# Kernel tuning notes

Measured on AMD Instinct MI355X. Metric: run time of the kernel, lower is better.

## Reference

```python
import jax, jax.numpy as jnp
import numpy as np

# Production-scale dims: tokens T = B*S = 1024, d_model = 768, 8 experts, top-2 routing
B, S, D, E, K = 1, 1024, 768, 8, 2
H = 4 * D  # expert hidden dim


def setup_inputs() -> dict:
    key = jax.random.key(0)
    ks = jax.random.split(key, 6)
    s = jnp.float32(0.02)
    return {
        "x": jax.random.normal(ks[0], (B, S, D), jnp.float32),
        "Wr": jax.random.normal(ks[1], (E, D), jnp.float32) * s,      # router Linear (no bias), torch layout [out,in]
        "W1": jax.random.normal(ks[2], (E, H, D), jnp.float32) * s,   # per-expert first Linear
        "b1": jnp.zeros((E, H), jnp.float32),
        "W2": jax.random.normal(ks[3], (E, D, H), jnp.float32) * s,   # per-expert second Linear
        "b2": jnp.zeros((E, D), jnp.float32),
        "sW1": jax.random.normal(ks[4], (H, D), jnp.float32) * s,     # shared expert
        "sb1": jnp.zeros((H,), jnp.float32),
        "sW2": jax.random.normal(ks[5], (D, H), jnp.float32) * s,
        "sb2": jnp.zeros((D,), jnp.float32),
    }


def reference(x, Wr, W1, b1, W2, b2, sW1, sb1, sW2, sb2):
    Bx, Sx, Dx = x.shape
    xf = x.reshape(-1, Dx)                                   # [T, D]
    T = xf.shape[0]

    # Router: top-k logits, others masked to -inf, then softmax.
    # softmax over -inf-masked logits == softmax over the k kept logits scattered back.
    logits = xf @ Wr.T                                       # [T, E]
    topv, idx = jax.lax.top_k(logits, K)                     # [T, K]
    gate_k = jax.nn.softmax(topv, axis=-1)                   # [T, K]
    gates = jnp.zeros((T, logits.shape[-1]), x.dtype).at[
        jnp.arange(T)[:, None], idx
    ].add(gate_k)                                            # [T, E], zero for unrouted experts

    # Expert MLPs (dense over experts; gate is exactly zero for unrouted -> same math
    # as the original masked gather/scatter loop). Dropout is identity in eval mode.
    h = jax.nn.relu(jnp.einsum('td,ehd->teh', xf, W1) + b1)  # [T, E, H]
    y = jnp.einsum('teh,edh->ted', h, W2) + b2               # [T, E, D]
    moe = jnp.einsum('te,ted->td', gates, y)                 # [T, D]

    # Shared expert: original adds 0.1 * shared(x) once per expert that selected the
    # token; every token is selected by exactly K (distinct top-k) experts.
    sh = jax.nn.relu(xf @ sW1.T + sb1) @ sW2.T + sb2         # [T, D]
    out = moe + (0.1 * K) * sh
    return out.reshape(Bx, Sx, Dx)
```

## Files before the change

kernel.cpp:

```cpp
#include <hip/hip_runtime.h>

#define T_TOK 1024
#define Dm 768
#define Hm 3072
#define NE 8
#define NPACK 3072
#define MAXTILES 32

typedef __attribute__((ext_vector_type(8))) short short8;
typedef __attribute__((ext_vector_type(4))) float f32x4;

__device__ __forceinline__ unsigned f2bf(float f) {
  unsigned u = __builtin_bit_cast(unsigned, f);
  u += 0x7fffu + ((u >> 16) & 1u);
  return u >> 16;
}
__device__ __forceinline__ unsigned pk2bf(float a, float b) {
  return f2bf(a) | (f2bf(b) << 16);
}
__device__ __forceinline__ float bf2f(unsigned short s) {
  unsigned u = ((unsigned)s) << 16;
  return __builtin_bit_cast(float, u);
}

__global__ __launch_bounds__(256) void router_kernel(
    const float* __restrict__ x, const float* __restrict__ Wr,
    int* __restrict__ counts, int* __restrict__ tlist,
    int4* __restrict__ tok2row, float2* __restrict__ tok2g) {
  __shared__ float sWr[NE * Dm];
  for (int i = threadIdx.x; i < NE * Dm; i += 256) sWr[i] = Wr[i];
  __syncthreads();
  const int wave = threadIdx.x >> 6, lane = threadIdx.x & 63;
  const int t = blockIdx.x * 4 + wave;
  float acc[NE];
#pragma unroll
  for (int e = 0; e < NE; e++) acc[e] = 0.f;
  for (int d = lane; d < Dm; d += 64) {
    float xv = x[t * Dm + d];
#pragma unroll
    for (int e = 0; e < NE; e++) acc[e] += xv * sWr[e * Dm + d];
  }
#pragma unroll
  for (int e = 0; e < NE; e++) {
#pragma unroll
    for (int off = 32; off > 0; off >>= 1) acc[e] += __shfl_down(acc[e], off);
  }
  if (lane == 0) {
    int i0 = 0; float v0 = acc[0];
#pragma unroll
    for (int e = 1; e < NE; e++) if (acc[e] > v0) { v0 = acc[e]; i0 = e; }
    int i1 = -1; float v1 = -1e30f;
#pragma unroll
    for (int e = 0; e < NE; e++) if (e != i0 && acc[e] > v1) { v1 = acc[e]; i1 = e; }
    float g0 = 1.f / (1.f + expf(v1 - v0));
    float g1 = 1.f - g0;
    int p0 = atomicAdd(&counts[i0], 1);
    tlist[i0 * T_TOK + p0] = t;
    int p1 = atomicAdd(&counts[i1], 1);
    tlist[i1 * T_TOK + p1] = t;
    tok2row[t] = make_int4(i0, p0, i1, p1);
    tok2g[t] = float2{g0, g1};
  }
}

template <int MODE>
__global__ __launch_bounds__(512) void moe_gemm(
    const float* __restrict__ x,
    const float* __restrict__ W1, const float* __restrict__ b1,
    const float* __restrict__ sW1, const float* __restrict__ sb1,
    const float* __restrict__ W2, const float* __restrict__ sW2,
    const float* __restrict__ sb2,
    unsigned short* __restrict__ hbuf, unsigned short* __restrict__ ybuf,
    float* __restrict__ outp,
    const int* __restrict__ counts, const int* __restrict__ tlist) {
  constexpr int BN    = (MODE == 0) ? 128 : 96;
  constexpr int Kfull = (MODE == 0) ? Dm : Hm;
  constexpr int NK    = Kfull / 64;
  constexpr int M_REP = (MODE == 0) ? 4 : 2;
  constexpr int N_REP = (MODE == 0) ? 2 : 3;
  constexpr int NBR   = BN / 32;

  const int b = blockIdx.x;
  int nIdx, ti;
  if constexpr (MODE == 0) { nIdx = (b % 8) + 8 * ((b / 8) % 3); ti = b / 24; }
  else                     { nIdx = b % 8;                        ti = b / 8;  }
  const int n0 = nIdx * BN;

  int e = 0, m0 = 0, pbase = 0, Ne = 0;
  bool found = false;
  for (int ee = 0; ee <= NE; ee++) {
    int ne = (ee < NE) ? counts[ee] : T_TOK;
    int nt = (ne + 127) >> 7;
    if (!found) {
      if (ti < nt) { e = ee; Ne = ne; m0 = ti << 7; found = true; }
      else { ti -= nt; pbase += ne; }
    }
  }
  if (!found) return;

  const float* Bw;
  const float* bias;
  if constexpr (MODE == 0) {
    Bw   = (e < NE) ? W1 + (size_t)e * Hm * Dm : sW1;
    bias = (e < NE) ? b1 + (size_t)e * Hm : sb1;
  } else {
    Bw   = (e < NE) ? W2 + (size_t)e * Dm * Hm : sW2;
    bias = sb2;
  }

  __shared__ unsigned short sA[128][72];
  __shared__ unsigned short sB[BN][72];

  const int tid = threadIdx.x;
  const int lane = tid & 63;
  const int wid = tid >> 6;
  int rb, cb;
  if constexpr (MODE == 0) { rb = (wid >> 2) * 64; cb = (wid & 3) * 32; }
  else                     { rb = (wid >> 1) * 32; cb = (wid & 1) * 48; }

  const float* aPtrF[4];
  const unsigned short* aPtrH[2];
  if constexpr (MODE == 0) {
#pragma unroll
    for (int c = 0; c < 4; c++) {
      int gi = m0 + c * 32 + (tid >> 4);
      int si = gi < Ne ? gi : Ne - 1;
      int tok = (e < NE) ? tlist[e * T_TOK + si] : si;
      aPtrF[c] = x + (size_t)tok * Dm + (tid & 15) * 4;
    }
  } else {
#pragma unroll
    for (int c = 0; c < 2; c++) {
      int prow = pbase + m0 + c * 64 + (tid >> 3);
      if (prow >= NPACK) prow = NPACK - 1;
      aPtrH[c] = hbuf + (size_t)prow * Hm + (tid & 7) * 8;
    }
  }
  const float* bPtrF[NBR];
#pragma unroll
  for (int c = 0; c < NBR; c++) {
    int nrow = n0 + c * 32 + (tid >> 4);
    bPtrF[c] = Bw + (size_t)nrow * Kfull + (tid & 15) * 4;
  }

  f32x4 acc[M_REP][N_REP];
#pragma unroll
  for (int m = 0; m < M_REP; m++)
#pragma unroll
    for (int n = 0; n < N_REP; n++) acc[m][n] = (f32x4)0.0f;

  const int rF = tid >> 4;
  const int cF = (tid & 15) * 4;
  const int rH = tid >> 3;
  const int cH = (tid & 7) * 8;
  const int frow = lane & 15;
  const int fk = (lane >> 4) * 8;

  float4 aFA[4], bFA[NBR], aFB[4], bFB[NBR];
  uint4 aHA[2], aHB[2];

  auto stage_load_A = [&](int ko) {
    if constexpr (MODE == 0) {
#pragma unroll
      for (int c = 0; c < 4; c++) aFA[c] = *(const float4*)(aPtrF[c] + ko);
    } else {
#pragma unroll
      for (int c = 0; c < 2; c++) aHA[c] = *(const uint4*)(aPtrH[c] + ko);
    }
#pragma unroll
    for (int c = 0; c < NBR; c++) bFA[c] = *(const float4*)(bPtrF[c] + ko);
  };
  auto stage_load_B = [&](int ko) {
    if constexpr (MODE == 0) {
#pragma unroll
      for (int c = 0; c < 4; c++) aFB[c] = *(const float4*)(aPtrF[c] + ko);
    } else {
#pragma unroll
      for (int c = 0; c < 2; c++) aHB[c] = *(const uint4*)(aPtrH[c] + ko);
    }
#pragma unroll
    for (int c = 0; c < NBR; c++) bFB[c] = *(const float4*)(bPtrF[c] + ko);
  };
  auto stage_write_A = [&]() {
    if constexpr (MODE == 0) {
#pragma unroll
      for (int c = 0; c < 4; c++)
        *(uint2*)&sA[c * 32 + rF][cF] =
            make_uint2(pk2bf(aFA[c].x, aFA[c].y), pk2bf(aFA[c].z, aFA[c].w));
    } else {
#pragma unroll
      for (int c = 0; c < 2; c++) *(uint4*)&sA[c * 64 + rH][cH] = aHA[c];
    }
#pragma unroll
    for (int c = 0; c < NBR; c++)
      *(uint2*)&sB[c * 32 + rF][cF] =
          make_uint2(pk2bf(bFA[c].x, bFA[c].y), pk2bf(bFA[c].z, bFA[c].w));
  };
  auto stage_write_B = [&]() {
    if constexpr (MODE == 0) {
#pragma unroll
      for (int c = 0; c < 4; c++)
        *(uint2*)&sA[c * 32 + rF][cF] =
            make_uint2(pk2bf(aFB[c].x, aFB[c].y), pk2bf(aFB[c].z, aFB[c].w));
    } else {
#pragma unroll
      for (int c = 0; c < 2; c++) *(uint4*)&sA[c * 64 + rH][cH] = aHB[c];
    }
#pragma unroll
    for (int c = 0; c < NBR; c++)
      *(uint2*)&sB[c * 32 + rF][cF] =
          make_uint2(pk2bf(bFB[c].x, bFB[c].y), pk2bf(bFB[c].z, bFB[c].w));
  };
  auto do_mfma = [&]() {
#pragma unroll
    for (int kk = 0; kk < 2; kk++) {
      short8 af[M_REP], bfr[N_REP];
#pragma unroll
      for (int m = 0; m < M_REP; m++)
        af[m] = *(const short8*)&sA[rb + m * 16 + frow][kk * 32 + fk];
#pragma unroll
      for (int n = 0; n < N_REP; n++)
        bfr[n] = *(const short8*)&sB[cb + n * 16 + frow][kk * 32 + fk];
#pragma unroll
      for (int m = 0; m < M_REP; m++)
#pragma unroll
        for (int n = 0; n < N_REP; n++)
          acc[m][n] = __builtin_amdgcn_mfma_f32_16x16x32_bf16(af[m], bfr[n], acc[m][n], 0, 0, 0);
    }
  };

  stage_load_A(0);
  stage_load_B(64);

  for (int ks = 0; ks < NK; ks += 2) {
    stage_write_A();
    __syncthreads();
    if (ks + 2 < NK) stage_load_A((ks + 2) * 64);
    do_mfma();
    __syncthreads();
    stage_write_B();
    __syncthreads();
    if (ks + 3 < NK) stage_load_B((ks + 3) * 64);
    do_mfma();
    __syncthreads();
  }

#pragma unroll
  for (int m = 0; m < M_REP; m++) {
    int lr = rb + m * 16 + (lane >> 4) * 4;
#pragma unroll
    for (int n = 0; n < N_REP; n++) {
      int gc = n0 + cb + n * 16 + (lane & 15);
#pragma unroll
      for (int j = 0; j < 4; j++) {
        int gi = m0 + lr + j;
        if (gi >= Ne) continue;
        float v = acc[m][n][j];
        if constexpr (MODE == 0) {
          v += bias[gc];
          v = v > 0.f ? v : 0.f;
          hbuf[(size_t)(pbase + gi) * Hm + gc] = (unsigned short)f2bf(v);
        } else {
          if (e < NE) {
            ybuf[(size_t)(pbase + gi) * Dm + gc] = (unsigned short)f2bf(v);
          } else {
            outp[(size_t)gi * Dm + gc] = 0.2f * (v + bias[gc]);
          }
        }
      }
    }
  }
}

__global__ __launch_bounds__(256) void finalize_kernel(
    const unsigned short* __restrict__ ybuf, const int* __restrict__ counts,
    const int4* __restrict__ tok2row, const float2* __restrict__ tok2g,
    const float* __restrict__ b2, float* __restrict__ out) {
  const int t = blockIdx.x;
  int bases[NE];
  int s = 0;
#pragma unroll
  for (int e = 0; e < NE; e++) { bases[e] = s; s += counts[e]; }
  const int4 rr = tok2row[t];
  const float2 gg = tok2g[t];
  const int r0 = bases[rr.x] + rr.y;
  const int r1 = bases[rr.z] + rr.w;
  for (int d = threadIdx.x; d < Dm; d += 256) {
    float v0 = bf2f(ybuf[(size_t)r0 * Dm + d]) + b2[rr.x * Dm + d];
    float v1 = bf2f(ybuf[(size_t)r1 * Dm + d]) + b2[rr.z * Dm + d];
    out[(size_t)t * Dm + d] += gg.x * v0 + gg.y * v1;
  }
}

extern "C" void kernel_launch(void* const* d_in, const int* in_sizes, int n_in,
                              void* d_out, int out_size, void* d_ws, size_t ws_size,
                              hipStream_t stream) {
  const float* x   = (const float*)d_in[0];
  const float* Wr  = (const float*)d_in[1];
  const float* W1  = (const float*)d_in[2];
  const float* b1  = (const float*)d_in[3];
  const float* W2  = (const float*)d_in[4];
  const float* b2  = (const float*)d_in[5];
  const float* sW1 = (const float*)d_in[6];
  const float* sb1 = (const float*)d_in[7];
  const float* sW2 = (const float*)d_in[8];
  const float* sb2 = (const float*)d_in[9];
  float* out = (float*)d_out;

  char* ws = (char*)d_ws;
  int*    counts  = (int*)(ws + 0);
  int4*   tok2row = (int4*)(ws + 128);
  float2* tok2g   = (float2*)(ws + 16512);
  int*    tlist   = (int*)(ws + 24704);
  unsigned short* hbuf = (unsigned short*)(ws + 57472);
  unsigned short* ybuf = (unsigned short*)(ws + 18931840);

  (void)hipMemsetAsync(counts, 0, 128, stream);

  router_kernel<<<dim3(T_TOK / 4), 256, 0, stream>>>(x, Wr, counts, tlist, tok2row, tok2g);

  moe_gemm<0><<<dim3(24 * MAXTILES), 512, 0, stream>>>(
      x, W1, b1, sW1, sb1, W2, sW2, sb2, hbuf, ybuf, out, counts, tlist);
  moe_gemm<1><<<dim3(8 * MAXTILES), 512, 0, stream>>>(
      x, W1, b1, sW1, sb1, W2, sW2, sb2, hbuf, ybuf, out, counts, tlist);

  finalize_kernel<<<dim3(T_TOK), 256, 0, stream>>>(ybuf, counts, tok2row, tok2g, b2, out);
}
```

Baseline: 356.6 us.

## Double-buffer LDS tiles in MoE GEMM to halve barriers per k-step

Shared-memory A/B tiles become two ping-pong buffers, so the next tile can be written to LDS while the current one is consumed by MFMA. Each k-tile now needs one barrier instead of two. A custom barrier macro waits only on LDS counters and adds a scheduling fence. LDS usage doubles, which may lower occupancy, and the hand-written waitcnt barrier relies on global loads being consumed before the LDS writes.

```diff
diff --git a/kernel.cpp b/kernel.cpp
--- a/kernel.cpp
+++ b/kernel.cpp
@@ -22,6 +22,13 @@
   unsigned u = ((unsigned)s) << 16;
   return __builtin_bit_cast(float, u);
 }
+
+#define SYNCB()                                            \
+  do {                                                     \
+    asm volatile("s_waitcnt lgkmcnt(0)" ::: "memory");     \
+    __builtin_amdgcn_s_barrier();                          \
+    __builtin_amdgcn_sched_barrier(0);                     \
+  } while (0)
 
 __global__ __launch_bounds__(256) void router_kernel(
     const float* __restrict__ x, const float* __restrict__ Wr,
@@ -75,7 +82,7 @@
     const int* __restrict__ counts, const int* __restrict__ tlist) {
   constexpr int BN    = (MODE == 0) ? 128 : 96;
   constexpr int Kfull = (MODE == 0) ? Dm : Hm;
-  constexpr int NK    = Kfull / 64;
+  constexpr int NT    = Kfull / 64;
   constexpr int M_REP = (MODE == 0) ? 4 : 2;
   constexpr int N_REP = (MODE == 0) ? 2 : 3;
   constexpr int NBR   = BN / 32;
@@ -108,8 +115,8 @@
     bias = sb2;
   }
 
-  __shared__ unsigned short sA[128][72];
-  __shared__ unsigned short sB[BN][72];
+  __shared__ unsigned short sA[2][128][72];
+  __shared__ unsigned short sB[2][BN][72];
 
   const int tid = threadIdx.x;
   const int lane = tid & 63;
@@ -159,7 +166,8 @@
   float4 aFA[4], bFA[NBR], aFB[4], bFB[NBR];
   uint4 aHA[2], aHB[2];
 
-  auto stage_load_A = [&](int ko) {
+  auto loadA = [&](int kt) {
+    int ko = kt * 64;
     if constexpr (MODE == 0) {
 #pragma unroll
       for (int c = 0; c < 4; c++) aFA[c] = *(const float4*)(aPtrF[c] + ko);
@@ -170,7 +178,8 @@
 #pragma unroll
     for (int c = 0; c < NBR; c++) bFA[c] = *(const float4*)(bPtrF[c] + ko);
   };
-  auto stage_load_B = [&](int ko) {
+  auto loadB = [&](int kt) {
+    int ko = kt * 64;
     if constexpr (MODE == 0) {
 #pragma unroll
       for (int c = 0; c < 4; c++) aFB[c] = *(const float4*)(aPtrF[c] + ko);
@@ -181,46 +190,46 @@
 #pragma unroll
     for (int c = 0; c < NBR; c++) bFB[c] = *(const float4*)(bPtrF[c] + ko);
   };
-  auto stage_write_A = [&]() {
+  auto writeLdsA = [&](int buf) {
     if constexpr (MODE == 0) {
 #pragma unroll
       for (int c = 0; c < 4; c++)
-        *(uint2*)&sA[c * 32 + rF][cF] =
+        *(uint2*)&sA[buf][c * 32 + rF][cF] =
             make_uint2(pk2bf(aFA[c].x, aFA[c].y), pk2bf(aFA[c].z, aFA[c].w));
     } else {
 #pragma unroll
-      for (int c = 0; c < 2; c++) *(uint4*)&sA[c * 64 + rH][cH] = aHA[c];
+      for (int c = 0; c < 2; c++) *(uint4*)&sA[buf][c * 64 + rH][cH] = aHA[c];
     }
 #pragma unroll
     for (int c = 0; c < NBR; c++)
-      *(uint2*)&sB[c * 32 + rF][cF] =
+      *(uint2*)&sB[buf][c * 32 + rF][cF] =
           make_uint2(pk2bf(bFA[c].x, bFA[c].y), pk2bf(bFA[c].z, bFA[c].w));
   };
-  auto stage_write_B = [&]() {
+  auto writeLdsB = [&](int buf) {
     if constexpr (MODE == 0) {
 #pragma unroll
       for (int c = 0; c < 4; c++)
-        *(uint2*)&sA[c * 32 + rF][cF] =
+        *(uint2*)&sA[buf][c * 32 + rF][cF] =
             make_uint2(pk2bf(aFB[c].x, aFB[c].y), pk2bf(aFB[c].z, aFB[c].w));
     } else {
 #pragma unroll
-      for (int c = 0; c < 2; c++) *(uint4*)&sA[c * 64 + rH][cH] = aHB[c];
+      for (int c = 0; c < 2; c++) *(uint4*)&sA[buf][c * 64 + rH][cH] = aHB[c];
     }
 #pragma unroll
     for (int c = 0; c < NBR; c++)
-      *(uint2*)&sB[c * 32 + rF][cF] =
+      *(uint2*)&sB[buf][c * 32 + rF][cF] =
           make_uint2(pk2bf(bFB[c].x, bFB[c].y), pk2bf(bFB[c].z, bFB[c].w));
   };
-  auto do_mfma = [&]() {
+  auto do_mfma = [&](int buf) {
 #pragma unroll
     for (int kk = 0; kk < 2; kk++) {
       short8 af[M_REP], bfr[N_REP];
 #pragma unroll
       for (int m = 0; m < M_REP; m++)
-        af[m] = *(const short8*)&sA[rb + m * 16 + frow][kk * 32 + fk];
+        af[m] = *(const short8*)&sA[buf][rb + m * 16 + frow][kk * 32 + fk];
 #pragma unroll
       for (int n = 0; n < N_REP; n++)
-        bfr[n] = *(const short8*)&sB[cb + n * 16 + frow][kk * 32 + fk];
+        bfr[n] = *(const short8*)&sB[buf][cb + n * 16 + frow][kk * 32 + fk];
 #pragma unroll
       for (int m = 0; m < M_REP; m++)
 #pragma unroll
@@ -229,20 +238,22 @@
     }
   };
 
-  stage_load_A(0);
-  stage_load_B(64);
-
-  for (int ks = 0; ks < NK; ks += 2) {
-    stage_write_A();
-    __syncthreads();
-    if (ks + 2 < NK) stage_load_A((ks + 2) * 64);
-    do_mfma();
-    __syncthreads();
-    stage_write_B();
-    __syncthreads();
-    if (ks + 3 < NK) stage_load_B((ks + 3) * 64);
-    do_mfma();
-    __syncthreads();
+  loadA(0);
+  loadB(1);
+  writeLdsA(0);
+  SYNCB();
+
+  for (int ks = 0; ks < NT; ks += 2) {
+    if (ks + 2 < NT) loadA(ks + 2);
+    do_mfma(0);
+    writeLdsB(1);
+    SYNCB();
+    if (ks + 3 < NT) loadB(ks + 3);
+    do_mfma(1);
+    if (ks + 2 < NT) {
+      writeLdsA(0);
+      SYNCB();
+    }
   }
 
 #pragma unroll
```

After: 361.3 us. About the same (+1.3%).
